# Optimization experiments

Hardware: AMD Instinct MI355X
Metric: run time of the kernel (lower is better)

The kernel has to match this reference:

```python
import jax, jax.numpy as jnp
import numpy as np

N, E, G = 50000, 800000, 128
IN, HID, HEAD = 1280, 256, 4
DH = HID // HEAD
EPS = 1e-5
ATT_SCALE = 1.0 / np.sqrt(1280.0).astype(np.float32)  # hardcoded in source


def _seg_softmax(x, seg, n):
    # softmax over segments along axis 0; x: [K] or [K, H]
    m = jax.ops.segment_max(x, seg, num_segments=n)
    e = jnp.exp(x - m[seg])
    s = jax.ops.segment_sum(e, seg, num_segments=n)
    return e / s[seg]


def _bn(x, g, b):
    # eval-mode BatchNorm1d with init running stats (mean=0, var=1)
    return g * x * (1.0 / np.sqrt(1.0 + EPS)) + b


def _ln(x, g, b):
    mu = x.mean(-1, keepdims=True)
    var = ((x - mu) ** 2).mean(-1, keepdims=True)
    return g * (x - mu) / jnp.sqrt(var + EPS) + b


def setup_inputs() -> dict:
    key = jax.random.key(0)
    ks = jax.random.split(key, 40)
    rn = lambda i, shp, s=0.05: jax.random.normal(ks[i], shp, jnp.float32) * s
    inp = {
        "h": jax.random.normal(ks[0], (N, IN), jnp.float32),
        "gcn_w0": rn(1, (IN, HID)), "gcn_b0": rn(2, (HID,), 0.01),
        "gcn_w1": rn(3, (HID, HID)), "gcn_b1": rn(4, (HID,), 0.01),
        "bn_gcn0_g": 1.0 + rn(5, (HID,), 0.1), "bn_gcn0_b": rn(6, (HID,), 0.01),
        "bn_gcn1_g": 1.0 + rn(7, (HID,), 0.1), "bn_gcn1_b": rn(8, (HID,), 0.01),
        "gat_w0": rn(9, (IN, HID)), "gat_al0": rn(10, (HEAD, DH)), "gat_ar0": rn(11, (HEAD, DH)), "gat_bias0": rn(12, (HID,), 0.01),
        "gat_w1": rn(13, (HID, HID)), "gat_al1": rn(14, (HEAD, DH)), "gat_ar1": rn(15, (HEAD, DH)), "gat_bias1": rn(16, (HID,), 0.01),
        "bn_gat0_g": 1.0 + rn(17, (HID,), 0.1), "bn_gat0_b": rn(18, (HID,), 0.01),
        "bn_gat1_g": 1.0 + rn(19, (HID,), 0.1), "bn_gat1_b": rn(20, (HID,), 0.01),
        "gate_w": rn(21, (2 * HID, HID)), "gate_b": rn(22, (HID,), 0.01),
        "qw": rn(23, (HEAD, HID, HID)), "kw": rn(24, (HEAD, HID, HID)), "vw": rn(25, (HEAD, HID, HID)),
        "ct_w": rn(26, (HEAD * HID, HID)),
        "ff_w1": rn(27, (HID, 2 * HID)), "ff_b1": rn(28, (2 * HID,), 0.01),
        "ff_w2": rn(29, (2 * HID, HID)), "ff_b2": rn(30, (HID,), 0.01),
        "ln_g": 1.0 + rn(31, (HID,), 0.1), "ln_b": rn(32, (HID,), 0.01),
        "src": jax.random.randint(ks[33], (E,), 0, N, jnp.int32),
        "dst": jax.random.randint(ks[34], (E,), 0, N, jnp.int32),
        "gid": jnp.sort(jax.random.randint(ks[35], (N,), 0, G, jnp.int32)),
        "num_graphs": G,
    }
    return inp


def reference(h, gcn_w0, gcn_b0, gcn_w1, gcn_b1, bn_gcn0_g, bn_gcn0_b, bn_gcn1_g, bn_gcn1_b,
              gat_w0, gat_al0, gat_ar0, gat_bias0, gat_w1, gat_al1, gat_ar1, gat_bias1,
              bn_gat0_g, bn_gat0_b, bn_gat1_g, bn_gat1_b, gate_w, gate_b,
              qw, kw, vw, ct_w, ff_w1, ff_b1, ff_w2, ff_b2, ln_g, ln_b,
              src, dst, gid, num_graphs):
    n = h.shape[0]
    ones_e = jnp.ones(src.shape[0], h.dtype)
    # dgl.mean_nodes per graph
    cnt = jnp.clip(jax.ops.segment_sum(jnp.ones(n, h.dtype), gid, num_segments=num_graphs), 1.0)
    init_avg_h = jax.ops.segment_sum(h, gid, num_segments=num_graphs) / cnt[:, None]
    # GraphConv norm='both', degrees clamped to >=1
    deg_out = jnp.clip(jax.ops.segment_sum(ones_e, src, num_segments=n), 1.0)
    deg_in = jnp.clip(jax.ops.segment_sum(ones_e, dst, num_segments=n), 1.0)
    ns, nd = deg_out ** -0.5, deg_in ** -0.5

    def gcn(x, w, b):
        m = (x * ns[:, None]) @ w  # [N, HID]
        return jax.ops.segment_sum(m[src], dst, num_segments=n) * nd[:, None] + b

    hg = jax.nn.relu(_bn(gcn(h, gcn_w0, gcn_b0), bn_gcn0_g, bn_gcn0_b))
    hg = jax.nn.relu(_bn(gcn(hg, gcn_w1, gcn_b1), bn_gcn1_g, bn_gcn1_b)) + hg

    def gat(x, w, al, ar, b):
        f = (x @ w).reshape(n, HEAD, DH)
        el = (f * al).sum(-1)  # [N, HEAD]
        er = (f * ar).sum(-1)
        e = jax.nn.leaky_relu(el[src] + er[dst], 0.2)  # [E, HEAD]
        alpha = _seg_softmax(e, dst, n)  # edge softmax over incoming edges
        out = jax.ops.segment_sum(alpha[:, :, None] * f[src], dst, num_segments=n)
        return out.reshape(n, HID) + b

    ha = jax.nn.elu(_bn(gat(h, gat_w0, gat_al0, gat_ar0, gat_bias0), bn_gat0_g, bn_gat0_b))
    ha = jax.nn.elu(_bn(gat(ha, gat_w1, gat_al1, gat_ar1, gat_bias1), bn_gat1_g, bn_gat1_b)) + ha

    gate = jax.nn.sigmoid(jnp.concatenate([hg, ha], axis=1) @ gate_w + gate_b)
    x = gate * hg + (1.0 - gate) * ha  # residue_h

    # transformer_block: per-graph node softmax attention
    q = jnp.einsum('nd,hde->nhe', x, qw)
    k = jnp.einsum('nd,hde->nhe', x, kw)
    v = jnp.einsum('nd,hde->nhe', x, vw)
    att = (q * k).sum(-1) * ATT_SCALE  # [N, HEAD]
    alpha = _seg_softmax(att, gid, num_graphs)  # dgl.softmax_nodes per head
    mo = (v * alpha[:, :, None]).reshape(n, HEAD * HID) @ ct_w
    x1 = _ln(mo + x, ln_g, ln_b)
    x2 = _ln(jax.nn.relu(x1 @ ff_w1 + ff_b1) @ ff_w2 + ff_b2 + x1, ln_g, ln_b)

    readout = jax.ops.segment_sum(x2, gid, num_segments=num_graphs)
    return readout, init_avg_h
```

## Files before the change

kernel.cpp:

```cpp
#include <hip/hip_runtime.h>

#define NN 50000
#define NE 800000
#define NG 128
#define DIN 1280
#define HIDDEN 256
#define BNS 0.9999950000374997f
#define ATT_SCALE 0.027950849718747373f
#define LN_EPS 1e-5f

typedef __attribute__((ext_vector_type(8))) short short8;
typedef __attribute__((ext_vector_type(4))) float floatx4;

__device__ __forceinline__ float b2f(unsigned short u) {
  return __uint_as_float(((unsigned int)u) << 16);
}
__device__ __forceinline__ unsigned short f2b(float f) {
  unsigned int x = __float_as_uint(f);
  x += 0x7fffu + ((x >> 16) & 1u);
  return (unsigned short)(x >> 16);
}

__global__ void transpose_w_k(const float* __restrict__ src, unsigned short* __restrict__ dst,
                              int K, int Nc) {
  int idx = blockIdx.x * 256 + threadIdx.x;
  if (idx >= K * Nc) return;
  int n = idx / K, k = idx % K;
  dst[idx] = f2b(src[(size_t)k * Nc + n]);
}

__global__ void mw_k(const float* __restrict__ qw, const float* __restrict__ kw,
                     unsigned short* __restrict__ dst) {
  int col = blockIdx.x;
  int d = threadIdx.x;
  int hh = col >> 8, dp = col & 255;
  const float* qr = qw + ((size_t)hh * 256 + d) * 256;
  const float* kr = kw + ((size_t)hh * 256 + dp) * 256;
  float s = 0.f;
  for (int e = 0; e < 256; e += 4) {
    float4 a = *(const float4*)(qr + e);
    float4 b = *(const float4*)(kr + e);
    s += a.x * b.x + a.y * b.y + a.z * b.z + a.w * b.w;
  }
  dst[(size_t)col * 256 + d] = f2b(s);
}

__global__ void v_transpose_k(const float* __restrict__ vw, unsigned short* __restrict__ dst) {
  int idx = blockIdx.x * 256 + threadIdx.x;
  if (idx >= 1024 * 256) return;
  int r = idx >> 8;
  int d = idx & 255;
  int hh = r >> 8;
  int e2 = r & 255;
  dst[(size_t)(1024 + r) * 256 + d] = f2b(vw[((size_t)hh * 256 + d) * 256 + e2]);
}

__global__ void cvt_avg_k(const float* __restrict__ h, const int* __restrict__ gid,
                          unsigned short* __restrict__ h_bf, float* __restrict__ out1) {
  int row0 = blockIdx.x * 50;
  int tid = threadIdx.x;
  float acc[5] = {0, 0, 0, 0, 0};
  int cur_g = gid[row0];
  for (int r = 0; r < 50; ++r) {
    int row = row0 + r;
    int g = gid[row];
    if (g != cur_g) {
#pragma unroll
      for (int j = 0; j < 5; ++j) {
        atomicAdd(&out1[(size_t)cur_g * DIN + j * 256 + tid], acc[j]);
        acc[j] = 0.f;
      }
      cur_g = g;
    }
#pragma unroll
    for (int j = 0; j < 5; ++j) {
      float v = h[(size_t)row * DIN + j * 256 + tid];
      acc[j] += v;
      h_bf[(size_t)row * DIN + j * 256 + tid] = f2b(v);
    }
  }
#pragma unroll
  for (int j = 0; j < 5; ++j)
    atomicAdd(&out1[(size_t)cur_g * DIN + j * 256 + tid], acc[j]);
}

__global__ void div_avg_k(const int* __restrict__ start, float* __restrict__ out1) {
  int idx = blockIdx.x * 256 + threadIdx.x;
  if (idx >= NG * DIN) return;
  int g = idx / DIN;
  float cnt = (float)(start[g + 1] - start[g]);
  if (cnt < 1.f) cnt = 1.f;
  out1[idx] /= cnt;
}

__global__ void graph_bounds_k(const int* __restrict__ gid, int* __restrict__ start, int n) {
  int i = blockIdx.x * 256 + threadIdx.x;
  if (i >= n) return;
  int g = gid[i];
  if (i == 0) {
    for (int gg = 0; gg <= g; ++gg) start[gg] = 0;
  } else {
    int gp = gid[i - 1];
    for (int gg = gp + 1; gg <= g; ++gg) start[gg] = i;
  }
  if (i == n - 1) {
    for (int gg = g + 1; gg <= NG; ++gg) start[gg] = n;
  }
}

__global__ void degrees_k(const int* __restrict__ src, const int* __restrict__ dst,
                          int* __restrict__ deg_out, int* __restrict__ deg_in, int e) {
  int i = blockIdx.x * 256 + threadIdx.x;
  if (i >= e) return;
  atomicAdd(&deg_out[src[i]], 1);
  atomicAdd(&deg_in[dst[i]], 1);
}

__global__ void invsqrt_k(const int* __restrict__ deg_out, const int* __restrict__ deg_in,
                          float* __restrict__ ns, float* __restrict__ nd, int n) {
  int i = blockIdx.x * 256 + threadIdx.x;
  if (i >= n) return;
  int a = deg_out[i]; if (a < 1) a = 1;
  int b = deg_in[i];  if (b < 1) b = 1;
  ns[i] = rsqrtf((float)a);
  nd[i] = rsqrtf((float)b);
}

__global__ void scan_local_k(const int* __restrict__ deg, int* __restrict__ row_ptr,
                             int* __restrict__ bsum) {
  __shared__ int buf[256];
  int b = blockIdx.x, t = threadIdx.x;
  int i = b * 256 + t;
  int v = (i < NN) ? deg[i] : 0;
  buf[t] = v;
  __syncthreads();
  for (int off = 1; off < 256; off <<= 1) {
    int tv = (t >= off) ? buf[t - off] : 0;
    __syncthreads();
    buf[t] += tv;
    __syncthreads();
  }
  if (i < NN) row_ptr[i] = buf[t] - v;
  if (t == 255) bsum[b] = buf[255];
}

__global__ void scan_bsum_k(int* __restrict__ bsum, int* __restrict__ boff, int nb,
                            int* __restrict__ row_ptr) {
  __shared__ int buf[256];
  int t = threadIdx.x;
  int v = (t < nb) ? bsum[t] : 0;
  buf[t] = v;
  __syncthreads();
  for (int off = 1; off < 256; off <<= 1) {
    int tv = (t >= off) ? buf[t - off] : 0;
    __syncthreads();
    buf[t] += tv;
    __syncthreads();
  }
  if (t < nb) boff[t] = buf[t] - v;
  if (t == 0) row_ptr[NN] = NE;
}

__global__ void scan_add_k(int* __restrict__ row_ptr, const int* __restrict__ boff) {
  int i = blockIdx.x * 256 + threadIdx.x;
  if (i >= NN) return;
  row_ptr[i] += boff[blockIdx.x];
}

__global__ void fill_csr_k(const int* __restrict__ src, const int* __restrict__ dst,
                           const int* __restrict__ row_ptr, int* __restrict__ fill,
                           int* __restrict__ csr_src, int e) {
  int i = blockIdx.x * 256 + threadIdx.x;
  if (i >= e) return;
  int d = dst[i];
  int pos = row_ptr[d] + atomicAdd(&fill[d], 1);
  csr_src[pos] = src[i];
}

template <int MODE>
__global__ __launch_bounds__(256, 2) void gemm_bf16(const unsigned short* __restrict__ A,
                                                    const unsigned short* __restrict__ Bt,
                                                    void* __restrict__ Cout,
                                                    const float* __restrict__ bias,
                                                    int M, int K, int Nc,
                                                    const unsigned short* __restrict__ xtile,
                                                    float* __restrict__ attp,
                                                    const float* __restrict__ ascale) {
  __shared__ unsigned short sbuf[16384];
  unsigned short* lA = sbuf;
  unsigned short* lB = sbuf + 8192;
  const int tid = threadIdx.x;
  const int n0 = blockIdx.x * 128;
  const int m0 = blockIdx.y * 128;
  const int w = tid >> 6;
  const int lane = tid & 63;
  const int wr = (w >> 1) * 64;
  const int wc = (w & 1) * 64;
  const int quad = lane >> 4;
  const int l15 = lane & 15;
  const int js = tid & 7;
  const int mbase = tid >> 3;
  const int wbase = w * 64;

  floatx4 acc[4][4];
#pragma unroll
  for (int i = 0; i < 4; ++i)
#pragma unroll
    for (int j = 0; j < 4; ++j) acc[i][j] = (floatx4)0.0f;

  for (int k0 = 0; k0 < K; k0 += 64) {
    __syncthreads();
    if (MODE == 5) {
#pragma unroll
      for (int it = 0; it < 4; ++it) {
        int m = it * 32 + mbase;
        int gm = m0 + m;
        if (gm >= M) gm = M - 1;
        uint4 va = *(const uint4*)(A + (size_t)gm * K + k0 + js * 8);
        float s = ascale[(size_t)gm * 4 + (k0 >> 8)];
        unsigned short* pp = (unsigned short*)&va;
#pragma unroll
        for (int c = 0; c < 8; ++c) pp[c] = f2b(b2f(pp[c]) * s);
        *(uint4*)(lA + (size_t)(m * 8 + (js ^ (m & 7))) * 8) = va;
      }
    } else {
#pragma unroll
      for (int it = 0; it < 4; ++it) {
        int c = it * 256 + wbase + lane;
        int m = c >> 3, g = c & 7;
        int gm = m0 + m;
        if (gm >= M) gm = M - 1;
        const unsigned short* gp = A + (size_t)gm * K + k0 + (g ^ (m & 7)) * 8;
        __builtin_amdgcn_global_load_lds(
            (const __attribute__((address_space(1))) unsigned int*)gp,
            (__attribute__((address_space(3))) unsigned int*)(lA + (size_t)(it * 256 + wbase) * 8),
            16, 0, 0);
      }
    }
#pragma unroll
    for (int it = 0; it < 4; ++it) {
      int c = it * 256 + wbase + lane;
      int m = c >> 3, g = c & 7;
      int gn = n0 + m;
      const unsigned short* gp = Bt + (size_t)gn * K + k0 + (g ^ (m & 7)) * 8;
      __builtin_amdgcn_global_load_lds(
          (const __attribute__((address_space(1))) unsigned int*)gp,
          (__attribute__((address_space(3))) unsigned int*)(lB + (size_t)(it * 256 + wbase) * 8),
          16, 0, 0);
    }
    __syncthreads();
#pragma unroll
    for (int ks = 0; ks < 2; ++ks) {
      int kb = ks * 4 + quad;
      short8 af[4], bfr[4];
#pragma unroll
      for (int ri = 0; ri < 4; ++ri) {
        int r = wr + ri * 16 + l15;
        af[ri] = *(const short8*)(lA + (size_t)(r * 8 + (kb ^ (r & 7))) * 8);
      }
#pragma unroll
      for (int ci = 0; ci < 4; ++ci) {
        int c = wc + ci * 16 + l15;
        bfr[ci] = *(const short8*)(lB + (size_t)(c * 8 + (kb ^ (c & 7))) * 8);
      }
#pragma unroll
      for (int ri = 0; ri < 4; ++ri)
#pragma unroll
        for (int ci = 0; ci < 4; ++ci)
          acc[ri][ci] = __builtin_amdgcn_mfma_f32_16x16x32_bf16(af[ri], bfr[ci], acc[ri][ci], 0, 0, 0);
    }
  }

  if (MODE == 4 && n0 < 1024) {
    __syncthreads();
    int cb = n0 & 255;
#pragma unroll
    for (int it2 = 0; it2 < 8; ++it2) {
      int linear = it2 * 256 + tid;
      int rr = linear >> 4;
      int c8 = (linear & 15) * 8;
      int gr = m0 + rr;
      if (gr >= M) gr = M - 1;
      *(uint4*)(sbuf + rr * 128 + c8) = *(const uint4*)(xtile + (size_t)gr * 256 + cb + c8);
    }
    __syncthreads();
    int head = n0 >> 8;
#pragma unroll
    for (int ri = 0; ri < 4; ++ri) {
      int lrow = wr + ri * 16 + quad * 4;
#pragma unroll
      for (int r = 0; r < 4; ++r) {
        float p = 0.f;
#pragma unroll
        for (int ci = 0; ci < 4; ++ci)
          p += acc[ri][ci][r] * b2f(sbuf[(lrow + r) * 128 + wc + ci * 16 + l15]);
        p += __shfl_xor(p, 1);
        p += __shfl_xor(p, 2);
        p += __shfl_xor(p, 4);
        p += __shfl_xor(p, 8);
        if (l15 == 0) {
          int grow = m0 + lrow + r;
          if (grow < M) atomicAdd(&attp[(size_t)grow * 4 + head], p * ATT_SCALE);
        }
      }
    }
    return;
  }

#pragma unroll
  for (int ri = 0; ri < 4; ++ri) {
    int row = m0 + wr + ri * 16 + quad * 4;
#pragma unroll
    for (int ci = 0; ci < 4; ++ci) {
      int col = n0 + wc + ci * 16 + l15;
      float bv = (MODE == 2) ? bias[col] : 0.f;
#pragma unroll
      for (int r = 0; r < 4; ++r) {
        if (row + r < M) {
          float v = acc[ri][ci][r];
          if (MODE == 2) { v += bv; v = fmaxf(v, 0.f); }
          if (MODE == 1)
            ((float*)Cout)[(size_t)(row + r) * Nc + col] = v;
          else if (MODE == 4)
            ((unsigned short*)Cout)[(size_t)(row + r) * 1024 + col - 1024] = f2b(v);
          else
            ((unsigned short*)Cout)[(size_t)(row + r) * Nc + col] = f2b(v);
        }
      }
    }
  }
}

__global__ void gcn_agg_k(const unsigned short* __restrict__ m, int ldm,
                          const int* __restrict__ row_ptr, const int* __restrict__ csr_src,
                          const float* __restrict__ ns, const float* __restrict__ nd,
                          const float* __restrict__ bias,
                          const float* __restrict__ bng, const float* __restrict__ bnb,
                          const unsigned short* __restrict__ resid, int ldr,
                          unsigned short* __restrict__ out, int ldo) {
  int node = blockIdx.x * 4 + (threadIdx.x >> 6);
  if (node >= NN) return;
  int lane = threadIdx.x & 63;
  int s = row_ptr[node], e = row_ptr[node + 1];
  float a0 = 0, a1 = 0, a2 = 0, a3 = 0;
  for (int i = s; i < e; ++i) {
    int u = csr_src[i];
    float w = ns[u];
    ushort4 v = *(const ushort4*)(m + (size_t)u * ldm + lane * 4);
    a0 += w * b2f(v.x); a1 += w * b2f(v.y); a2 += w * b2f(v.z); a3 += w * b2f(v.w);
  }
  float ndv = nd[node];
  int col = lane * 4;
  float vals[4] = {a0, a1, a2, a3};
  ushort4 o;
#pragma unroll
  for (int c = 0; c < 4; ++c) {
    float v = vals[c] * ndv + bias[col + c];
    v = bng[col + c] * v * BNS + bnb[col + c];
    v = fmaxf(v, 0.f);
    if (resid) v += b2f(resid[(size_t)node * ldr + col + c]);
    ((unsigned short*)&o)[c] = f2b(v);
  }
  *(ushort4*)(out + (size_t)node * ldo + col) = o;
}

__global__ void elr_k(const unsigned short* __restrict__ f, int ldf,
                      const float* __restrict__ al, const float* __restrict__ ar,
                      float* __restrict__ elr) {
  int node = blockIdx.x * 4 + (threadIdx.x >> 6);
  if (node >= NN) return;
  int lane = threadIdx.x & 63;
  int head = lane >> 4;
  int col = lane * 4;
  int dcol = col & 63;
  ushort4 v = *(const ushort4*)(f + (size_t)node * ldf + col);
  float pl = 0, pr = 0;
#pragma unroll
  for (int c = 0; c < 4; ++c) {
    float x = b2f(((unsigned short*)&v)[c]);
    pl += x * al[head * 64 + dcol + c];
    pr += x * ar[head * 64 + dcol + c];
  }
#pragma unroll
  for (int off = 1; off < 16; off <<= 1) {
    pl += __shfl_xor(pl, off);
    pr += __shfl_xor(pr, off);
  }
  if ((lane & 15) == 0) {
    elr[(size_t)node * 8 + head] = pl;
    elr[(size_t)node * 8 + 4 + head] = pr;
  }
}

__global__ void gat_agg_k(const unsigned short* __restrict__ f, int ldf,
                          const int* __restrict__ row_ptr, const int* __restrict__ csr_src,
                          const float* __restrict__ elr,
                          const float* __restrict__ bias,
                          const float* __restrict__ bng, const float* __restrict__ bnb,
                          const unsigned short* __restrict__ resid, int ldr,
                          unsigned short* __restrict__ out, int ldo) {
  int node = blockIdx.x * 4 + (threadIdx.x >> 6);
  if (node >= NN) return;
  int lane = threadIdx.x & 63;
  int s = row_ptr[node], e = row_ptr[node + 1];
  float4 er = *(const float4*)(elr + (size_t)node * 8 + 4);
  float m0 = -1e30f, m1 = -1e30f, m2 = -1e30f, m3 = -1e30f;
  for (int i = s + lane; i < e; i += 64) {
    int u = csr_src[i];
    float4 el = *(const float4*)(elr + (size_t)u * 8);
    float t;
    t = el.x + er.x; t = t > 0.f ? t : 0.2f * t; m0 = fmaxf(m0, t);
    t = el.y + er.y; t = t > 0.f ? t : 0.2f * t; m1 = fmaxf(m1, t);
    t = el.z + er.z; t = t > 0.f ? t : 0.2f * t; m2 = fmaxf(m2, t);
    t = el.w + er.w; t = t > 0.f ? t : 0.2f * t; m3 = fmaxf(m3, t);
  }
#pragma unroll
  for (int off = 1; off < 64; off <<= 1) {
    m0 = fmaxf(m0, __shfl_xor(m0, off));
    m1 = fmaxf(m1, __shfl_xor(m1, off));
    m2 = fmaxf(m2, __shfl_xor(m2, off));
    m3 = fmaxf(m3, __shfl_xor(m3, off));
  }
  float s0 = 0, s1 = 0, s2 = 0, s3 = 0;
  for (int i = s + lane; i < e; i += 64) {
    int u = csr_src[i];
    float4 el = *(const float4*)(elr + (size_t)u * 8);
    float t;
    t = el.x + er.x; t = t > 0.f ? t : 0.2f * t; s0 += expf(t - m0);
    t = el.y + er.y; t = t > 0.f ? t : 0.2f * t; s1 += expf(t - m1);
    t = el.z + er.z; t = t > 0.f ? t : 0.2f * t; s2 += expf(t - m2);
    t = el.w + er.w; t = t > 0.f ? t : 0.2f * t; s3 += expf(t - m3);
  }
#pragma unroll
  for (int off = 1; off < 64; off <<= 1) {
    s0 += __shfl_xor(s0, off);
    s1 += __shfl_xor(s1, off);
    s2 += __shfl_xor(s2, off);
    s3 += __shfl_xor(s3, off);
  }
  int head = lane >> 4;
  float erh = head == 0 ? er.x : head == 1 ? er.y : head == 2 ? er.z : er.w;
  float mh = head == 0 ? m0 : head == 1 ? m1 : head == 2 ? m2 : m3;
  float sh = head == 0 ? s0 : head == 1 ? s1 : head == 2 ? s2 : s3;
  float inv_sh = (sh > 0.f) ? 1.f / sh : 0.f;
  float a0 = 0, a1 = 0, a2 = 0, a3 = 0;
  for (int i = s; i < e; ++i) {
    int u = csr_src[i];
    float t = elr[(size_t)u * 8 + head] + erh;
    t = t > 0.f ? t : 0.2f * t;
    float wgt = expf(t - mh) * inv_sh;
    ushort4 v = *(const ushort4*)(f + (size_t)u * ldf + lane * 4);
    a0 += wgt * b2f(v.x); a1 += wgt * b2f(v.y); a2 += wgt * b2f(v.z); a3 += wgt * b2f(v.w);
  }
  int col = lane * 4;
  float vals[4] = {a0, a1, a2, a3};
  ushort4 o;
#pragma unroll
  for (int c = 0; c < 4; ++c) {
    float v = vals[c] + bias[col + c];
    v = bng[col + c] * v * BNS + bnb[col + c];
    v = (v > 0.f) ? v : (expf(v) - 1.f);
    if (resid) v += b2f(resid[(size_t)node * ldr + col + c]);
    ((unsigned short*)&o)[c] = f2b(v);
  }
  *(ushort4*)(out + (size_t)node * ldo + col) = o;
}

__global__ void combine_k(const unsigned short* __restrict__ glogit, const float* __restrict__ gate_b,
                          const unsigned short* __restrict__ xcat,
                          unsigned short* __restrict__ xb) {
  int idx = blockIdx.x * 256 + threadIdx.x;
  if (idx >= NN * 64) return;
  int node = idx >> 6;
  int c = (idx & 63) * 4;
  ushort4 gl = *(const ushort4*)(glogit + (size_t)node * HIDDEN + c);
  ushort4 hgv = *(const ushort4*)(xcat + (size_t)node * 512 + c);
  ushort4 hav = *(const ushort4*)(xcat + (size_t)node * 512 + 256 + c);
  ushort4 ob;
  float g;
  g = 1.f / (1.f + expf(-(b2f(gl.x) + gate_b[c + 0]))); ob.x = f2b(g * b2f(hgv.x) + (1.f - g) * b2f(hav.x));
  g = 1.f / (1.f + expf(-(b2f(gl.y) + gate_b[c + 1]))); ob.y = f2b(g * b2f(hgv.y) + (1.f - g) * b2f(hav.y));
  g = 1.f / (1.f + expf(-(b2f(gl.z) + gate_b[c + 2]))); ob.z = f2b(g * b2f(hgv.z) + (1.f - g) * b2f(hav.z));
  g = 1.f / (1.f + expf(-(b2f(gl.w) + gate_b[c + 3]))); ob.w = f2b(g * b2f(hgv.w) + (1.f - g) * b2f(hav.w));
  *(ushort4*)(xb + (size_t)node * HIDDEN + c) = ob;
}

__global__ void gsoftmax_k(const float* __restrict__ att, const int* __restrict__ start,
                           float* __restrict__ alpha) {
  int g = blockIdx.x;
  int s = start[g], e = start[g + 1];
  int tid = threadIdx.x;
  __shared__ float red[256];
  __shared__ float mh[4], sh[4];
  float lm[4] = {-1e30f, -1e30f, -1e30f, -1e30f};
  for (int i = s + tid; i < e; i += 256) {
    float4 a = *(const float4*)(att + (size_t)i * 4);
    lm[0] = fmaxf(lm[0], a.x); lm[1] = fmaxf(lm[1], a.y);
    lm[2] = fmaxf(lm[2], a.z); lm[3] = fmaxf(lm[3], a.w);
  }
#pragma unroll
  for (int h = 0; h < 4; ++h) {
    red[tid] = lm[h]; __syncthreads();
    for (int off = 128; off > 0; off >>= 1) {
      if (tid < off) red[tid] = fmaxf(red[tid], red[tid + off]);
      __syncthreads();
    }
    if (tid == 0) mh[h] = red[0];
    __syncthreads();
  }
  float ls[4] = {0, 0, 0, 0};
  for (int i = s + tid; i < e; i += 256) {
    float4 a = *(const float4*)(att + (size_t)i * 4);
    ls[0] += expf(a.x - mh[0]); ls[1] += expf(a.y - mh[1]);
    ls[2] += expf(a.z - mh[2]); ls[3] += expf(a.w - mh[3]);
  }
#pragma unroll
  for (int h = 0; h < 4; ++h) {
    red[tid] = ls[h]; __syncthreads();
    for (int off = 128; off > 0; off >>= 1) {
      if (tid < off) red[tid] += red[tid + off];
      __syncthreads();
    }
    if (tid == 0) sh[h] = red[0];
    __syncthreads();
  }
  for (int i = s + tid; i < e; i += 256) {
    float4 a = *(const float4*)(att + (size_t)i * 4);
    float4 o;
    o.x = expf(a.x - mh[0]) / sh[0];
    o.y = expf(a.y - mh[1]) / sh[1];
    o.z = expf(a.z - mh[2]) / sh[2];
    o.w = expf(a.w - mh[3]) / sh[3];
    *(float4*)(alpha + (size_t)i * 4) = o;
  }
}

__global__ void ln1_k(const unsigned short* __restrict__ mo, const unsigned short* __restrict__ x,
                      const float* __restrict__ g, const float* __restrict__ b,
                      unsigned short* __restrict__ x1) {
  int node = blockIdx.x * 4 + (threadIdx.x >> 6);
  if (node >= NN) return;
  int lane = threadIdx.x & 63;
  int c = lane * 4;
  ushort4 a = *(const ushort4*)(mo + (size_t)node * HIDDEN + c);
  ushort4 xx = *(const ushort4*)(x + (size_t)node * HIDDEN + c);
  float v0 = b2f(a.x) + b2f(xx.x), v1 = b2f(a.y) + b2f(xx.y);
  float v2 = b2f(a.z) + b2f(xx.z), v3 = b2f(a.w) + b2f(xx.w);
  float sm = v0 + v1 + v2 + v3;
#pragma unroll
  for (int off = 1; off < 64; off <<= 1) sm += __shfl_xor(sm, off);
  float mu = sm * (1.f / 256.f);
  float d0 = v0 - mu, d1 = v1 - mu, d2 = v2 - mu, d3 = v3 - mu;
  float sq = d0 * d0 + d1 * d1 + d2 * d2 + d3 * d3;
#pragma unroll
  for (int off = 1; off < 64; off <<= 1) sq += __shfl_xor(sq, off);
  float inv = rsqrtf(sq * (1.f / 256.f) + LN_EPS);
  ushort4 ob;
  ob.x = f2b(g[c + 0] * d0 * inv + b[c + 0]);
  ob.y = f2b(g[c + 1] * d1 * inv + b[c + 1]);
  ob.z = f2b(g[c + 2] * d2 * inv + b[c + 2]);
  ob.w = f2b(g[c + 3] * d3 * inv + b[c + 3]);
  *(ushort4*)(x1 + (size_t)node * HIDDEN + c) = ob;
}

__global__ void ln2_k(const unsigned short* __restrict__ ff2o, const float* __restrict__ ffb2,
                      const unsigned short* __restrict__ x1,
                      const float* __restrict__ g, const float* __restrict__ b,
                      unsigned short* __restrict__ x2) {
  int node = blockIdx.x * 4 + (threadIdx.x >> 6);
  if (node >= NN) return;
  int lane = threadIdx.x & 63;
  int c = lane * 4;
  ushort4 a = *(const ushort4*)(ff2o + (size_t)node * HIDDEN + c);
  ushort4 xx = *(const ushort4*)(x1 + (size_t)node * HIDDEN + c);
  float v0 = b2f(a.x) + ffb2[c + 0] + b2f(xx.x), v1 = b2f(a.y) + ffb2[c + 1] + b2f(xx.y);
  float v2 = b2f(a.z) + ffb2[c + 2] + b2f(xx.z), v3 = b2f(a.w) + ffb2[c + 3] + b2f(xx.w);
  float sm = v0 + v1 + v2 + v3;
#pragma unroll
  for (int off = 1; off < 64; off <<= 1) sm += __shfl_xor(sm, off);
  float mu = sm * (1.f / 256.f);
  float d0 = v0 - mu, d1 = v1 - mu, d2 = v2 - mu, d3 = v3 - mu;
  float sq = d0 * d0 + d1 * d1 + d2 * d2 + d3 * d3;
#pragma unroll
  for (int off = 1; off < 64; off <<= 1) sq += __shfl_xor(sq, off);
  float inv = rsqrtf(sq * (1.f / 256.f) + LN_EPS);
  ushort4 ob;
  ob.x = f2b(g[c + 0] * d0 * inv + b[c + 0]);
  ob.y = f2b(g[c + 1] * d1 * inv + b[c + 1]);
  ob.z = f2b(g[c + 2] * d2 * inv + b[c + 2]);
  ob.w = f2b(g[c + 3] * d3 * inv + b[c + 3]);
  *(ushort4*)(x2 + (size_t)node * HIDDEN + c) = ob;
}

__global__ void readout_k(const unsigned short* __restrict__ x2, const int* __restrict__ start,
                          float* __restrict__ out0) {
  int g = blockIdx.x;
  int c = threadIdx.x;
  float acc = 0.f;
  for (int i = start[g]; i < start[g + 1]; ++i) acc += b2f(x2[(size_t)i * HIDDEN + c]);
  out0[(size_t)g * HIDDEN + c] = acc;
}

static const size_t OFF_BUFA   = 0;
static const size_t OFF_C01    = 128000000;
static const size_t OFF_HG0    = 179200000;
static const size_t OFF_HA0    = 204800000;
static const size_t OFF_M1     = 230400000;
static const size_t OFF_F1     = 256000000;
static const size_t OFF_XCAT   = 281600000;
static const size_t OFF_GLOGIT = 332800000;
static const size_t OFF_XB     = 358400000;
static const size_t OFF_MO     = 384000000;
static const size_t OFF_X1     = 409600000;
static const size_t OFF_ATT    = 435200000;
static const size_t OFF_ALPHA  = OFF_ATT + 800000;
static const size_t OFF_ELR0   = OFF_ALPHA + 800000;
static const size_t OFF_ELR1   = OFF_ELR0 + 1600000;
static const size_t OFF_START  = OFF_ELR1 + 1600000;
static const size_t OFF_DEGO   = OFF_START + 1024;
static const size_t OFF_DEGI   = OFF_DEGO + 200704;
static const size_t OFF_NS     = OFF_DEGI + 200704;
static const size_t OFF_ND     = OFF_NS + 200704;
static const size_t OFF_ROWP   = OFF_ND + 200704;
static const size_t OFF_FILL   = OFF_ROWP + 200704;
static const size_t OFF_BSUM   = OFF_FILL + 200704;
static const size_t OFF_BOFF   = OFF_BSUM + 1024;
static const size_t OFF_CSRS   = OFF_BOFF + 1024;
static const size_t OFF_W01T   = OFF_CSRS + 3200000;
static const size_t OFF_W1T    = OFF_W01T + 1310720;
static const size_t OFF_W1GT   = OFF_W1T + 131072;
static const size_t OFF_GATEWT = OFF_W1GT + 131072;
static const size_t OFF_WMVT   = OFF_GATEWT + 262144;
static const size_t OFF_CTWT   = OFF_WMVT + 1048576;
static const size_t OFF_FFW1T  = OFF_CTWT + 524288;
static const size_t OFF_FFW2T  = OFF_FFW1T + 262144;
static const size_t WS_NEED    = OFF_FFW2T + 262144;

extern "C" void kernel_launch(void* const* d_in, const int* in_sizes, int n_in,
                              void* d_out, int out_size, void* d_ws, size_t ws_size,
                              hipStream_t stream) {
  if (ws_size < WS_NEED) return;

  const float* h       = (const float*)d_in[0];
  const float* gcn_w0  = (const float*)d_in[1];
  const float* gcn_b0  = (const float*)d_in[2];
  const float* gcn_w1  = (const float*)d_in[3];
  const float* gcn_b1  = (const float*)d_in[4];
  const float* bn_gcn0_g = (const float*)d_in[5];
  const float* bn_gcn0_b = (const float*)d_in[6];
  const float* bn_gcn1_g = (const float*)d_in[7];
  const float* bn_gcn1_b = (const float*)d_in[8];
  const float* gat_w0  = (const float*)d_in[9];
  const float* gat_al0 = (const float*)d_in[10];
  const float* gat_ar0 = (const float*)d_in[11];
  const float* gat_bias0 = (const float*)d_in[12];
  const float* gat_w1  = (const float*)d_in[13];
  const float* gat_al1 = (const float*)d_in[14];
  const float* gat_ar1 = (const float*)d_in[15];
  const float* gat_bias1 = (const float*)d_in[16];
  const float* bn_gat0_g = (const float*)d_in[17];
  const float* bn_gat0_b = (const float*)d_in[18];
  const float* bn_gat1_g = (const float*)d_in[19];
  const float* bn_gat1_b = (const float*)d_in[20];
  const float* gate_w  = (const float*)d_in[21];
  const float* gate_b  = (const float*)d_in[22];
  const float* qw      = (const float*)d_in[23];
  const float* kw      = (const float*)d_in[24];
  const float* vw      = (const float*)d_in[25];
  const float* ct_w    = (const float*)d_in[26];
  const float* ff_w1   = (const float*)d_in[27];
  const float* ff_b1   = (const float*)d_in[28];
  const float* ff_w2   = (const float*)d_in[29];
  const float* ff_b2   = (const float*)d_in[30];
  const float* ln_g    = (const float*)d_in[31];
  const float* ln_b    = (const float*)d_in[32];
  const int* srcv = (const int*)d_in[33];
  const int* dstv = (const int*)d_in[34];
  const int* gid  = (const int*)d_in[35];

  char* ws = (char*)d_ws;
  unsigned short* h_bf = (unsigned short*)(ws + OFF_BUFA);
  unsigned short* yv   = (unsigned short*)(ws + OFF_BUFA);
  unsigned short* ff1o = (unsigned short*)(ws + OFF_BUFA);
  unsigned short* ff2o = (unsigned short*)(ws + OFF_BUFA + 51200000);
  unsigned short* x2   = (unsigned short*)(ws + OFF_BUFA + 76800000);
  unsigned short* c01  = (unsigned short*)(ws + OFF_C01);
  unsigned short* hg0  = (unsigned short*)(ws + OFF_HG0);
  unsigned short* ha0  = (unsigned short*)(ws + OFF_HA0);
  unsigned short* m1   = (unsigned short*)(ws + OFF_M1);
  unsigned short* f1   = (unsigned short*)(ws + OFF_F1);
  unsigned short* xcat = (unsigned short*)(ws + OFF_XCAT);
  unsigned short* glogit = (unsigned short*)(ws + OFF_GLOGIT);
  unsigned short* xb   = (unsigned short*)(ws + OFF_XB);
  unsigned short* mo   = (unsigned short*)(ws + OFF_MO);
  unsigned short* x1   = (unsigned short*)(ws + OFF_X1);
  float* att           = (float*)(ws + OFF_ATT);
  float* alpha         = (float*)(ws + OFF_ALPHA);
  float* elr0          = (float*)(ws + OFF_ELR0);
  float* elr1          = (float*)(ws + OFF_ELR1);
  int* start   = (int*)(ws + OFF_START);
  int* deg_out = (int*)(ws + OFF_DEGO);
  int* deg_in  = (int*)(ws + OFF_DEGI);
  float* ns    = (float*)(ws + OFF_NS);
  float* nd    = (float*)(ws + OFF_ND);
  int* row_ptr = (int*)(ws + OFF_ROWP);
  int* fill    = (int*)(ws + OFF_FILL);
  int* bsum    = (int*)(ws + OFF_BSUM);
  int* boff    = (int*)(ws + OFF_BOFF);
  int* csr_src = (int*)(ws + OFF_CSRS);
  unsigned short* w01t   = (unsigned short*)(ws + OFF_W01T);
  unsigned short* w1t    = (unsigned short*)(ws + OFF_W1T);
  unsigned short* w1gt   = (unsigned short*)(ws + OFF_W1GT);
  unsigned short* gatewt = (unsigned short*)(ws + OFF_GATEWT);
  unsigned short* wmvt   = (unsigned short*)(ws + OFF_WMVT);
  unsigned short* ctwt   = (unsigned short*)(ws + OFF_CTWT);
  unsigned short* ffw1t  = (unsigned short*)(ws + OFF_FFW1T);
  unsigned short* ffw2t  = (unsigned short*)(ws + OFF_FFW2T);

  float* out0 = (float*)d_out;
  float* out1 = out0 + NG * HIDDEN;

  hipMemsetAsync(deg_out, 0, NN * 4, stream);
  hipMemsetAsync(deg_in, 0, NN * 4, stream);
  hipMemsetAsync(fill, 0, NN * 4, stream);
  hipMemsetAsync(out1, 0, NG * DIN * 4, stream);
  hipMemsetAsync(att, 0, NN * 4 * 4, stream);

  transpose_w_k<<<(1280 * 256 + 255) / 256, 256, 0, stream>>>(gcn_w0, w01t, 1280, 256);
  transpose_w_k<<<(1280 * 256 + 255) / 256, 256, 0, stream>>>(gat_w0, w01t + 256 * 1280, 1280, 256);
  transpose_w_k<<<(256 * 256 + 255) / 256, 256, 0, stream>>>(gcn_w1, w1t, 256, 256);
  transpose_w_k<<<(256 * 256 + 255) / 256, 256, 0, stream>>>(gat_w1, w1gt, 256, 256);
  transpose_w_k<<<(512 * 256 + 255) / 256, 256, 0, stream>>>(gate_w, gatewt, 512, 256);
  mw_k<<<1024, 256, 0, stream>>>(qw, kw, wmvt);
  v_transpose_k<<<1024, 256, 0, stream>>>(vw, wmvt);
  transpose_w_k<<<(1024 * 256 + 255) / 256, 256, 0, stream>>>(ct_w, ctwt, 1024, 256);
  transpose_w_k<<<(256 * 512 + 255) / 256, 256, 0, stream>>>(ff_w1, ffw1t, 256, 512);
  transpose_w_k<<<(512 * 256 + 255) / 256, 256, 0, stream>>>(ff_w2, ffw2t, 512, 256);

  graph_bounds_k<<<(NN + 255) / 256, 256, 0, stream>>>(gid, start, NN);
  degrees_k<<<(NE + 255) / 256, 256, 0, stream>>>(srcv, dstv, deg_out, deg_in, NE);
  invsqrt_k<<<(NN + 255) / 256, 256, 0, stream>>>(deg_out, deg_in, ns, nd, NN);
  const int NB_SCAN = (NN + 255) / 256;
  scan_local_k<<<NB_SCAN, 256, 0, stream>>>(deg_in, row_ptr, bsum);
  scan_bsum_k<<<1, 256, 0, stream>>>(bsum, boff, NB_SCAN, row_ptr);
  scan_add_k<<<NB_SCAN, 256, 0, stream>>>(row_ptr, boff);
  fill_csr_k<<<(NE + 255) / 256, 256, 0, stream>>>(srcv, dstv, row_ptr, fill, csr_src, NE);

  cvt_avg_k<<<NN / 50, 256, 0, stream>>>(h, gid, h_bf, out1);
  div_avg_k<<<(NG * DIN + 255) / 256, 256, 0, stream>>>(start, out1);

  const int MB = (NN + 127) / 128;
  gemm_bf16<0><<<dim3(4, MB), 256, 0, stream>>>(h_bf, w01t, c01, nullptr, NN, 1280, 512,
                                                nullptr, nullptr, nullptr);
  gcn_agg_k<<<NN / 4, 256, 0, stream>>>(c01, 512, row_ptr, csr_src, ns, nd,
                                        gcn_b0, bn_gcn0_g, bn_gcn0_b, nullptr, 0, hg0, 256);
  elr_k<<<NN / 4, 256, 0, stream>>>(c01 + 256, 512, gat_al0, gat_ar0, elr0);
  gat_agg_k<<<NN / 4, 256, 0, stream>>>(c01 + 256, 512, row_ptr, csr_src, elr0,
                                        gat_bias0, bn_gat0_g, bn_gat0_b, nullptr, 0, ha0, 256);
  gemm_bf16<0><<<dim3(2, MB), 256, 0, stream>>>(hg0, w1t, m1, nullptr, NN, 256, 256,
                                                nullptr, nullptr, nullptr);
  gcn_agg_k<<<NN / 4, 256, 0, stream>>>(m1, 256, row_ptr, csr_src, ns, nd,
                                        gcn_b1, bn_gcn1_g, bn_gcn1_b, hg0, 256, xcat, 512);
  gemm_bf16<0><<<dim3(2, MB), 256, 0, stream>>>(ha0, w1gt, f1, nullptr, NN, 256, 256,
                                                nullptr, nullptr, nullptr);
  elr_k<<<NN / 4, 256, 0, stream>>>(f1, 256, gat_al1, gat_ar1, elr1);
  gat_agg_k<<<NN / 4, 256, 0, stream>>>(f1, 256, row_ptr, csr_src, elr1,
                                        gat_bias1, bn_gat1_g, bn_gat1_b, ha0, 256, xcat + 256, 512);
  gemm_bf16<0><<<dim3(2, MB), 256, 0, stream>>>(xcat, gatewt, glogit, nullptr, NN, 512, 256,
                                                nullptr, nullptr, nullptr);
  combine_k<<<NN / 4, 256, 0, stream>>>(glogit, gate_b, xcat, xb);
  gemm_bf16<4><<<dim3(16, MB), 256, 0, stream>>>(xb, wmvt, yv, nullptr, NN, 256, 2048,
                                                 xb, att, nullptr);
  gsoftmax_k<<<NG, 256, 0, stream>>>(att, start, alpha);
  gemm_bf16<5><<<dim3(2, MB), 256, 0, stream>>>(yv, ctwt, mo, nullptr, NN, 1024, 256,
                                                nullptr, nullptr, alpha);
  ln1_k<<<NN / 4, 256, 0, stream>>>(mo, xb, ln_g, ln_b, x1);
  gemm_bf16<2><<<dim3(4, MB), 256, 0, stream>>>(x1, ffw1t, ff1o, ff_b1, NN, 256, 512,
                                                nullptr, nullptr, nullptr);
  gemm_bf16<0><<<dim3(2, MB), 256, 0, stream>>>(ff1o, ffw2t, ff2o, nullptr, NN, 512, 256,
                                                nullptr, nullptr, nullptr);
  ln2_k<<<NN / 4, 256, 0, stream>>>(ff2o, ff_b2, x1, ln_g, ln_b, x2);
  readout_k<<<NG, 256, 0, stream>>>(x2, start, out0);
}
```

Baseline: 1.671 ms.

## Fold V projection into output weights and fuse gate combine into GEMM epilogue

Precomputes W2 = Vw·ct_w per head so the attention output GEMM reads the 256-wide x tile, scaled per head by alpha, instead of materialising the 1024-wide V projection. The QK GEMM then only computes attention logits (1024 columns instead of 2048) and no longer writes yv. The gate sigmoid and combine step move into a new GEMM epilogue mode, which removes the combine kernel and the glogit buffer. In exchange there is an extra weight-setup matmul, and the folded product is rounded to bf16, which may change numerics slightly.

```diff
diff --git a/kernel.cpp b/kernel.cpp
--- a/kernel.cpp
+++ b/kernel.cpp
@@ -45,14 +45,16 @@
   dst[(size_t)col * 256 + d] = f2b(s);
 }
 
-__global__ void v_transpose_k(const float* __restrict__ vw, unsigned short* __restrict__ dst) {
-  int idx = blockIdx.x * 256 + threadIdx.x;
-  if (idx >= 1024 * 256) return;
-  int r = idx >> 8;
-  int d = idx & 255;
-  int hh = r >> 8;
-  int e2 = r & 255;
-  dst[(size_t)(1024 + r) * 256 + d] = f2b(vw[((size_t)hh * 256 + d) * 256 + e2]);
+__global__ void w2_k(const float* __restrict__ vw, const float* __restrict__ ctw,
+                     unsigned short* __restrict__ dst) {
+  int b = blockIdx.x;
+  int c = threadIdx.x;
+  int hh = b >> 8, d = b & 255;
+  const float* vr = vw + ((size_t)hh * 256 + d) * 256;
+  float s = 0.f;
+  for (int e = 0; e < 256; ++e)
+    s += vr[e] * ctw[(size_t)(hh * 256 + e) * 256 + c];
+  dst[(size_t)c * 1024 + b] = f2b(s);
 }
 
 __global__ void cvt_avg_k(const float* __restrict__ h, const int* __restrict__ gid,
@@ -210,13 +212,13 @@
 
   for (int k0 = 0; k0 < K; k0 += 64) {
     __syncthreads();
-    if (MODE == 5) {
+    if (MODE == 6) {
 #pragma unroll
       for (int it = 0; it < 4; ++it) {
         int m = it * 32 + mbase;
         int gm = m0 + m;
         if (gm >= M) gm = M - 1;
-        uint4 va = *(const uint4*)(A + (size_t)gm * K + k0 + js * 8);
+        uint4 va = *(const uint4*)(A + (size_t)gm * 256 + (k0 & 255) + js * 8);
         float s = ascale[(size_t)gm * 4 + (k0 >> 8)];
         unsigned short* pp = (unsigned short*)&va;
 #pragma unroll
@@ -271,7 +273,7 @@
     }
   }
 
-  if (MODE == 4 && n0 < 1024) {
+  if (MODE == 4) {
     __syncthreads();
     int cb = n0 & 255;
 #pragma unroll
@@ -307,6 +309,28 @@
     return;
   }
 
+  if (MODE == 7) {
+#pragma unroll
+    for (int ri = 0; ri < 4; ++ri) {
+      int row = m0 + wr + ri * 16 + quad * 4;
+#pragma unroll
+      for (int ci = 0; ci < 4; ++ci) {
+        int col = n0 + wc + ci * 16 + l15;
+        float bv = bias[col];
+#pragma unroll
+        for (int r = 0; r < 4; ++r) {
+          if (row + r < M) {
+            float g = 1.f / (1.f + expf(-(acc[ri][ci][r] + bv)));
+            float hg = b2f(xtile[(size_t)(row + r) * 512 + col]);
+            float ha = b2f(xtile[(size_t)(row + r) * 512 + 256 + col]);
+            ((unsigned short*)Cout)[(size_t)(row + r) * Nc + col] = f2b(g * hg + (1.f - g) * ha);
+          }
+        }
+      }
+    }
+    return;
+  }
+
 #pragma unroll
   for (int ri = 0; ri < 4; ++ri) {
     int row = m0 + wr + ri * 16 + quad * 4;
@@ -321,8 +345,6 @@
           if (MODE == 2) { v += bv; v = fmaxf(v, 0.f); }
           if (MODE == 1)
             ((float*)Cout)[(size_t)(row + r) * Nc + col] = v;
-          else if (MODE == 4)
-            ((unsigned short*)Cout)[(size_t)(row + r) * 1024 + col - 1024] = f2b(v);
           else
             ((unsigned short*)Cout)[(size_t)(row + r) * Nc + col] = f2b(v);
         }
@@ -464,25 +486,6 @@
     ((unsigned short*)&o)[c] = f2b(v);
   }
   *(ushort4*)(out + (size_t)node * ldo + col) = o;
-}
-
-__global__ void combine_k(const unsigned short* __restrict__ glogit, const float* __restrict__ gate_b,
-                          const unsigned short* __restrict__ xcat,
-                          unsigned short* __restrict__ xb) {
-  int idx = blockIdx.x * 256 + threadIdx.x;
-  if (idx >= NN * 64) return;
-  int node = idx >> 6;
-  int c = (idx & 63) * 4;
-  ushort4 gl = *(const ushort4*)(glogit + (size_t)node * HIDDEN + c);
-  ushort4 hgv = *(const ushort4*)(xcat + (size_t)node * 512 + c);
-  ushort4 hav = *(const ushort4*)(xcat + (size_t)node * 512 + 256 + c);
-  ushort4 ob;
-  float g;
-  g = 1.f / (1.f + expf(-(b2f(gl.x) + gate_b[c + 0]))); ob.x = f2b(g * b2f(hgv.x) + (1.f - g) * b2f(hav.x));
-  g = 1.f / (1.f + expf(-(b2f(gl.y) + gate_b[c + 1]))); ob.y = f2b(g * b2f(hgv.y) + (1.f - g) * b2f(hav.y));
-  g = 1.f / (1.f + expf(-(b2f(gl.z) + gate_b[c + 2]))); ob.z = f2b(g * b2f(hgv.z) + (1.f - g) * b2f(hav.z));
-  g = 1.f / (1.f + expf(-(b2f(gl.w) + gate_b[c + 3]))); ob.w = f2b(g * b2f(hgv.w) + (1.f - g) * b2f(hav.w));
-  *(ushort4*)(xb + (size_t)node * HIDDEN + c) = ob;
 }
 
 __global__ void gsoftmax_k(const float* __restrict__ att, const int* __restrict__ start,
@@ -680,7 +683,6 @@
 
   char* ws = (char*)d_ws;
   unsigned short* h_bf = (unsigned short*)(ws + OFF_BUFA);
-  unsigned short* yv   = (unsigned short*)(ws + OFF_BUFA);
   unsigned short* ff1o = (unsigned short*)(ws + OFF_BUFA);
   unsigned short* ff2o = (unsigned short*)(ws + OFF_BUFA + 51200000);
   unsigned short* x2   = (unsigned short*)(ws + OFF_BUFA + 76800000);
@@ -690,7 +692,6 @@
   unsigned short* m1   = (unsigned short*)(ws + OFF_M1);
   unsigned short* f1   = (unsigned short*)(ws + OFF_F1);
   unsigned short* xcat = (unsigned short*)(ws + OFF_XCAT);
-  unsigned short* glogit = (unsigned short*)(ws + OFF_GLOGIT);
   unsigned short* xb   = (unsigned short*)(ws + OFF_XB);
   unsigned short* mo   = (unsigned short*)(ws + OFF_MO);
   unsigned short* x1   = (unsigned short*)(ws + OFF_X1);
@@ -713,7 +714,7 @@
   unsigned short* w1gt   = (unsigned short*)(ws + OFF_W1GT);
   unsigned short* gatewt = (unsigned short*)(ws + OFF_GATEWT);
   unsigned short* wmvt   = (unsigned short*)(ws + OFF_WMVT);
-  unsigned short* ctwt   = (unsigned short*)(ws + OFF_CTWT);
+  unsigned short* w2t    = (unsigned short*)(ws + OFF_CTWT);
   unsigned short* ffw1t  = (unsigned short*)(ws + OFF_FFW1T);
   unsigned short* ffw2t  = (unsigned short*)(ws + OFF_FFW2T);
 
@@ -732,8 +733,7 @@
   transpose_w_k<<<(256 * 256 + 255) / 256, 256, 0, stream>>>(gat_w1, w1gt, 256, 256);
   transpose_w_k<<<(512 * 256 + 255) / 256, 256, 0, stream>>>(gate_w, gatewt, 512, 256);
   mw_k<<<1024, 256, 0, stream>>>(qw, kw, wmvt);
-  v_transpose_k<<<1024, 256, 0, stream>>>(vw, wmvt);
-  transpose_w_k<<<(1024 * 256 + 255) / 256, 256, 0, stream>>>(ct_w, ctwt, 1024, 256);
+  w2_k<<<1024, 256, 0, stream>>>(vw, ct_w, w2t);
   transpose_w_k<<<(256 * 512 + 255) / 256, 256, 0, stream>>>(ff_w1, ffw1t, 256, 512);
   transpose_w_k<<<(512 * 256 + 255) / 256, 256, 0, stream>>>(ff_w2, ffw2t, 512, 256);
 
@@ -766,13 +766,12 @@
   elr_k<<<NN / 4, 256, 0, stream>>>(f1, 256, gat_al1, gat_ar1, elr1);
   gat_agg_k<<<NN / 4, 256, 0, stream>>>(f1, 256, row_ptr, csr_src, elr1,
                                         gat_bias1, bn_gat1_g, bn_gat1_b, ha0, 256, xcat + 256, 512);
-  gemm_bf16<0><<<dim3(2, MB), 256, 0, stream>>>(xcat, gatewt, glogit, nullptr, NN, 512, 256,
-                                                nullptr, nullptr, nullptr);
-  combine_k<<<NN / 4, 256, 0, stream>>>(glogit, gate_b, xcat, xb);
-  gemm_bf16<4><<<dim3(16, MB), 256, 0, stream>>>(xb, wmvt, yv, nullptr, NN, 256, 2048,
-                                                 xb, att, nullptr);
+  gemm_bf16<7><<<dim3(2, MB), 256, 0, stream>>>(xcat, gatewt, xb, gate_b, NN, 512, 256,
+                                                xcat, nullptr, nullptr);
+  gemm_bf16<4><<<dim3(8, MB), 256, 0, stream>>>(xb, wmvt, nullptr, nullptr, NN, 256, 1024,
+                                                xb, att, nullptr);
   gsoftmax_k<<<NG, 256, 0, stream>>>(att, start, alpha);
-  gemm_bf16<5><<<dim3(2, MB), 256, 0, stream>>>(yv, ctwt, mo, nullptr, NN, 1024, 256,
+  gemm_bf16<6><<<dim3(2, MB), 256, 0, stream>>>(xb, w2t, mo, nullptr, NN, 1024, 256,
                                                 nullptr, nullptr, alpha);
   ln1_k<<<NN / 4, 256, 0, stream>>>(mo, xb, ln_g, ln_b, x1);
   gemm_bf16<2><<<dim3(4, MB), 256, 0, stream>>>(x1, ffw1t, ff1o, ff_b1, NN, 256, 512,
```

Result: no change. 1.664 ms (-0.4%).
